# Optimization experiments

Hardware: AMD Instinct MI355X
Metric: run time of the kernel (lower is better)

## Reference

```python
import jax, jax.numpy as jnp
import numpy as np

QB = 127.0  # 2**(8-1) - 1


def ternary_dequant(w):
    # absmean ternary quantization, then dequantize by scale
    scale = jnp.mean(jnp.abs(w))
    w_t = jnp.clip(jnp.round(w / (scale + 1e-8)), -1.0, 1.0)
    w_t = jnp.where(scale == 0.0, jnp.zeros_like(w), w_t)
    return w_t * scale


def activation_quantize(x):
    # per-row (last-dim) absmax int8 fake-quant
    scale = jnp.max(jnp.abs(x), axis=-1, keepdims=True) / QB
    scale = jnp.maximum(scale, 1e-8)
    return jnp.clip(jnp.round(x / scale), -QB, QB) * scale


def setup_inputs() -> dict:
    key = jax.random.key(0)
    kx, kw = jax.random.split(key)
    x = jax.random.normal(kx, (2, 4096, 4096), dtype=jnp.float32)
    # kaiming_uniform-ish init scale; exact init distribution is irrelevant to the math
    bound = 1.0 / np.sqrt(4096)
    weight = jax.random.uniform(kw, (4096, 4096), dtype=jnp.float32,
                                minval=-bound, maxval=bound)
    return {"x": x, "weight": weight}


def reference(x, weight):
    w_q = ternary_dequant(weight)        # [out, in]
    x_q = activation_quantize(x)         # [b, s, in]
    return jnp.einsum('bsi,oi->bso', x_q, w_q)
```

## Files before the change

### kernel.cpp

```cpp
#include <hip/hip_runtime.h>
#include <stdint.h>
#include <stddef.h>


#define K_DIM 4096
#define M_DIM 8192
#define N_DIM 4096

typedef int v4i __attribute__((ext_vector_type(4)));

__device__ __forceinline__ void async_copy16(void* lds, const void* g) {
  __builtin_amdgcn_global_load_lds(
      (const __attribute__((address_space(1))) unsigned int*)g,
      (__attribute__((address_space(3))) unsigned int*)lds,
      16, 0, 0);
}

__global__ void k_wsum(const float* __restrict__ w, double* __restrict__ partials) {
  const float4* w4 = (const float4*)w;
  int tid = blockIdx.x * 256 + threadIdx.x;
  double s = 0.0;
  for (int i = tid; i < 4194304; i += 262144) {
    float4 v = w4[i];
    s += (double)fabsf(v.x) + (double)fabsf(v.y) +
         (double)fabsf(v.z) + (double)fabsf(v.w);
  }
  for (int off = 32; off > 0; off >>= 1) s += __shfl_down(s, off);
  __shared__ double lsum[4];
  int lane = threadIdx.x & 63, wid = threadIdx.x >> 6;
  if (lane == 0) lsum[wid] = s;
  __syncthreads();
  if (threadIdx.x == 0)
    partials[blockIdx.x] = lsum[0] + lsum[1] + lsum[2] + lsum[3];
}

__global__ void k_wq(const float* __restrict__ w, const double* __restrict__ partials,
                     float* __restrict__ wscale, char* __restrict__ qw) {
  __shared__ float sT;
  if (threadIdx.x < 64) {
    double s = 0.0;
    for (int i = threadIdx.x; i < 1024; i += 64) s += partials[i];
    for (int off = 32; off > 0; off >>= 1) s += __shfl_down(s, off);
    if (threadIdx.x == 0) {
      float sc = (float)(s / 16777216.0);
      if (blockIdx.x == 0) *wscale = sc;
      float d = sc + 1e-8f;
      unsigned lo = 1u, hi = __float_as_uint(d);
      while (hi - lo > 1u) {
        unsigned mid = lo + ((hi - lo) >> 1);
        if (__uint_as_float(mid) / d > 0.5f) hi = mid; else lo = mid;
      }
      sT = __uint_as_float(hi);
    }
  }
  __syncthreads();
  const float T = sT;
  const float4* w4 = (const float4*)w;
  int* q4 = (int*)qw;
  int tid = blockIdx.x * 256 + threadIdx.x;
  for (int i = tid; i < 4194304; i += 524288) {
    float4 v = w4[i];
    int a = (int)(v.x >= T) - (int)(v.x <= -T);
    int b = (int)(v.y >= T) - (int)(v.y <= -T);
    int c = (int)(v.z >= T) - (int)(v.z <= -T);
    int e = (int)(v.w >= T) - (int)(v.w <= -T);
    q4[i] = (a & 255) | ((b & 255) << 8) | ((c & 255) << 16) | ((e & 255) << 24);
  }
}

__global__ void k_xq(const float* __restrict__ x, char* __restrict__ qx,
                     float* __restrict__ sx) {
  int row = blockIdx.x;
  const float4* xr = (const float4*)(x + (size_t)row * K_DIM);
  float4 v[4];
  float m = 0.f;
#pragma unroll
  for (int c = 0; c < 4; c++) {
    v[c] = xr[threadIdx.x + c * 256];
    m = fmaxf(m, fmaxf(fmaxf(fabsf(v[c].x), fabsf(v[c].y)),
                       fmaxf(fabsf(v[c].z), fabsf(v[c].w))));
  }
  for (int off = 32; off > 0; off >>= 1) m = fmaxf(m, __shfl_down(m, off));
  __shared__ float lm[4];
  __shared__ float bscale;
  int lane = threadIdx.x & 63, wid = threadIdx.x >> 6;
  if (lane == 0) lm[wid] = m;
  __syncthreads();
  if (threadIdx.x == 0) {
    float mm = fmaxf(fmaxf(lm[0], lm[1]), fmaxf(lm[2], lm[3]));
    float sc = fmaxf(mm / 127.0f, 1e-8f);
    bscale = sc;
    sx[row] = sc;
  }
  __syncthreads();
  float sc = bscale;
  int* q4 = (int*)(qx + (size_t)row * K_DIM);
#pragma unroll
  for (int c = 0; c < 4; c++) {
    int a = (int)fmaxf(fminf(rintf(v[c].x / sc), 127.f), -127.f);
    int b = (int)fmaxf(fminf(rintf(v[c].y / sc), 127.f), -127.f);
    int cc = (int)fmaxf(fminf(rintf(v[c].z / sc), 127.f), -127.f);
    int e = (int)fmaxf(fminf(rintf(v[c].w / sc), 127.f), -127.f);
    q4[threadIdx.x + c * 256] = (a & 255) | ((b & 255) << 8) | ((cc & 255) << 16) | ((e & 255) << 24);
  }
}

__global__ __launch_bounds__(512, 2) void k_gemm(const char* __restrict__ qx,
                       const char* __restrict__ qw,
                       const float* __restrict__ sx,
                       const float* __restrict__ wscale,
                       float* __restrict__ out) {
  __shared__ char lds[4][32768];

  const int tid = threadIdx.x;
  const int lane = tid & 63;
  const int wave = tid >> 6;
  const int wr = wave >> 2;
  const int wc = wave & 3;

  const int wg = (blockIdx.x & 7) * 64 + (blockIdx.x >> 3);
  const int bm = wg >> 4;
  const int bn = wg & 15;
  const int rowBase = bm * 256;
  const int colBase = bn * 256;

  const int rl = tid >> 2;
  const int kswz = (((tid & 3) ^ ((rl >> 1) & 3)) << 4);
  const char* gA0 = qx + (size_t)(rowBase + rl) * K_DIM + kswz;
  const char* gA1 = gA0 + (size_t)128 * K_DIM;
  const char* gB0 = qw + (size_t)(colBase + rl) * K_DIM + kswz;
  const char* gB1 = gB0 + (size_t)128 * K_DIM;
  const int dOff = wave << 10;

  const int sR = ((lane & 15) >> 1) & 3;
  const int kro = (((lane >> 4) ^ sR) << 4);
  const int aOff = ((wr << 7) + (lane & 15)) * 64 + kro;
  const int bOff = 16384 + ((wc << 6) + (lane & 15)) * 64 + kro;

  v4i acc[8][4] = {};

  auto STAGE = [&](int t) {
    char* b = &lds[t & 3][0];
    const size_t ko = (size_t)t << 6;
    async_copy16(b + dOff,         gA0 + ko);
    async_copy16(b + 8192 + dOff,  gA1 + ko);
    async_copy16(b + 16384 + dOff, gB0 + ko);
    async_copy16(b + 24576 + dOff, gB1 + ko);
  };

  v4i afA[4], bfA[4], afB[4], bfB[4];

#define PRE_READ(T, AF, BF)                                                  \
  {                                                                          \
    const char* bx_ = &lds[(T) & 3][0];                                      \
    _Pragma("unroll") for (int j_ = 0; j_ < 4; ++j_)                         \
        BF[j_] = *(const v4i*)(bx_ + bOff + j_ * 1024);                      \
    _Pragma("unroll") for (int j_ = 0; j_ < 4; ++j_)                         \
        AF[j_] = *(const v4i*)(bx_ + aOff + j_ * 1024);                      \
  }

#define FULL_ITER(T, CURAF, CURBF, NXTAF, NXTBF, DO_STAGE, VMC)              \
  {                                                                          \
    asm volatile("s_waitcnt vmcnt(" #VMC ")" ::: "memory");                  \
    __builtin_amdgcn_s_barrier();                                            \
    asm volatile("" ::: "memory");                                           \
    const char* bc_ = &lds[(T) & 3][0];                                      \
    v4i afL_[4];                                                             \
    _Pragma("unroll") for (int j_ = 0; j_ < 4; ++j_)                         \
        afL_[j_] = *(const v4i*)(bc_ + aOff + (4 + j_) * 1024);              \
    PRE_READ((T) + 1, NXTAF, NXTBF);                                         \
    if (DO_STAGE) STAGE((T) + 3);                                            \
    asm volatile("" ::: "memory");                                           \
    __builtin_amdgcn_s_setprio(1);                                           \
    _Pragma("unroll") for (int m_ = 0; m_ < 4; ++m_)                         \
        _Pragma("unroll") for (int n_ = 0; n_ < 4; ++n_)                     \
            acc[m_][n_] = __builtin_amdgcn_mfma_i32_16x16x64_i8(             \
                CURAF[m_], CURBF[n_], acc[m_][n_], 0, 0, 0);                 \
    _Pragma("unroll") for (int m_ = 0; m_ < 4; ++m_)                         \
        _Pragma("unroll") for (int n_ = 0; n_ < 4; ++n_)                     \
            acc[4 + m_][n_] = __builtin_amdgcn_mfma_i32_16x16x64_i8(         \
                afL_[m_], CURBF[n_], acc[4 + m_][n_], 0, 0, 0);              \
    __builtin_amdgcn_s_setprio(0);                                           \
  }

  STAGE(0); STAGE(1); STAGE(2);
  asm volatile("s_waitcnt vmcnt(8)" ::: "memory");
  __builtin_amdgcn_s_barrier();
  asm volatile("" ::: "memory");
  PRE_READ(0, afA, bfA);

  for (int tp = 0; tp < 30; ++tp) {
    const int t = tp * 2;
    FULL_ITER(t,     afA, bfA, afB, bfB, 1, 4);
    FULL_ITER(t + 1, afB, bfB, afA, bfA, 1, 4);
  }
  FULL_ITER(60, afA, bfA, afB, bfB, 1, 4);
  FULL_ITER(61, afB, bfB, afA, bfA, 0, 4);
  FULL_ITER(62, afA, bfA, afB, bfB, 0, 0);
  {
    const char* bc_ = &lds[63 & 3][0];
    v4i afL_[4];
#pragma unroll
    for (int j_ = 0; j_ < 4; ++j_)
      afL_[j_] = *(const v4i*)(bc_ + aOff + (4 + j_) * 1024);
    __builtin_amdgcn_s_setprio(1);
#pragma unroll
    for (int m_ = 0; m_ < 4; ++m_)
#pragma unroll
      for (int n_ = 0; n_ < 4; ++n_)
        acc[m_][n_] = __builtin_amdgcn_mfma_i32_16x16x64_i8(
            afB[m_], bfB[n_], acc[m_][n_], 0, 0, 0);
#pragma unroll
    for (int m_ = 0; m_ < 4; ++m_)
#pragma unroll
      for (int n_ = 0; n_ < 4; ++n_)
        acc[4 + m_][n_] = __builtin_amdgcn_mfma_i32_16x16x64_i8(
            afL_[m_], bfB[n_], acc[4 + m_][n_], 0, 0, 0);
    __builtin_amdgcn_s_setprio(0);
  }
#undef FULL_ITER
#undef PRE_READ

  const float swv = *wscale;
  const int col0 = colBase + (wc << 6) + (lane & 15);
  const int row0 = rowBase + (wr << 7) + ((lane >> 4) << 2);
#pragma unroll
  for (int m = 0; m < 8; ++m) {
#pragma unroll
    for (int r = 0; r < 4; ++r) {
      const int row = row0 + m * 16 + r;
      const float s = sx[row] * swv;
#pragma unroll
      for (int n = 0; n < 4; ++n)
        out[(size_t)row * N_DIM + col0 + n * 16] = (float)acc[m][n][r] * s;
    }
  }
}

extern "C" void kernel_launch(void* const* d_in, const int* in_sizes, int n_in,
                              void* d_out, int out_size, void* d_ws, size_t ws_size,
                              hipStream_t stream) {
  const float* x = (const float*)d_in[0];
  const float* w = (const float*)d_in[1];
  float* out = (float*)d_out;
  char* ws = (char*)d_ws;

  double* partials = (double*)ws;
  float* wscale    = (float*)(ws + 8192);
  float* sx        = (float*)(ws + 8448);
  char*  qw        = ws + 41472;
  char*  qx        = ws + 41472 + 16777216;

  k_wsum<<<1024, 256, 0, stream>>>(w, partials);
  k_wq  <<<2048, 256, 0, stream>>>(w, partials, wscale, qw);
  k_xq  <<<8192, 256, 0, stream>>>(x, qx, sx);
  k_gemm<<<32 * 16, 512, 0, stream>>>(qx, qw, sx, wscale, out);
}
```

Measured before the change: 396.0 us.

## Load A fragments directly from global into registers, stage only B in LDS

The GEMM stops staging the activation (A) tile through LDS. Each wave now loads its A fragments straight from global memory into registers one k-step ahead, and only the weight (B) tile is streamed into LDS asynchronously. The wave layout changes from 2x4 to 4x2 so each wave owns 64 rows by 128 columns, reading 8 B fragments from LDS per step. This halves LDS footprint and LDS read traffic, but A loads become uncoalesced 16-byte per-lane global reads with less latency hiding, and the vmcnt accounting mixes the A loads with the async B copies.

```diff
diff --git a/kernel.cpp b/kernel.cpp
--- a/kernel.cpp
+++ b/kernel.cpp
@@ -110,13 +110,13 @@
                        const float* __restrict__ sx,
                        const float* __restrict__ wscale,
                        float* __restrict__ out) {
-  __shared__ char lds[4][32768];
+  __shared__ char lds[4][16384];
 
   const int tid = threadIdx.x;
   const int lane = tid & 63;
   const int wave = tid >> 6;
-  const int wr = wave >> 2;
-  const int wc = wave & 3;
+  const int wr = wave >> 1;
+  const int wc = wave & 1;
 
   const int wg = (blockIdx.x & 7) * 64 + (blockIdx.x >> 3);
   const int bm = wg >> 4;
@@ -126,112 +126,88 @@
 
   const int rl = tid >> 2;
   const int kswz = (((tid & 3) ^ ((rl >> 1) & 3)) << 4);
-  const char* gA0 = qx + (size_t)(rowBase + rl) * K_DIM + kswz;
-  const char* gA1 = gA0 + (size_t)128 * K_DIM;
   const char* gB0 = qw + (size_t)(colBase + rl) * K_DIM + kswz;
   const char* gB1 = gB0 + (size_t)128 * K_DIM;
   const int dOff = wave << 10;
 
   const int sR = ((lane & 15) >> 1) & 3;
   const int kro = (((lane >> 4) ^ sR) << 4);
-  const int aOff = ((wr << 7) + (lane & 15)) * 64 + kro;
-  const int bOff = 16384 + ((wc << 6) + (lane & 15)) * 64 + kro;
-
-  v4i acc[8][4] = {};
-
-  auto STAGE = [&](int t) {
+  const int bOff = ((wc << 7) + (lane & 15)) * 64 + kro;
+
+  const char* gAf = qx + (size_t)(rowBase + (wr << 6) + (lane & 15)) * K_DIM
+                       + ((lane >> 4) << 4);
+
+  v4i acc[4][8] = {};
+  v4i aA[4], aB[4];
+
+  auto STAGE_B = [&](int t) {
     char* b = &lds[t & 3][0];
     const size_t ko = (size_t)t << 6;
-    async_copy16(b + dOff,         gA0 + ko);
-    async_copy16(b + 8192 + dOff,  gA1 + ko);
-    async_copy16(b + 16384 + dOff, gB0 + ko);
-    async_copy16(b + 24576 + dOff, gB1 + ko);
+    async_copy16(b + dOff,        gB0 + ko);
+    async_copy16(b + 8192 + dOff, gB1 + ko);
   };
 
-  v4i afA[4], bfA[4], afB[4], bfB[4];
-
-#define PRE_READ(T, AF, BF)                                                  \
+#define A_LOAD(T, DST)                                                       \
   {                                                                          \
-    const char* bx_ = &lds[(T) & 3][0];                                      \
-    _Pragma("unroll") for (int j_ = 0; j_ < 4; ++j_)                         \
-        BF[j_] = *(const v4i*)(bx_ + bOff + j_ * 1024);                      \
-    _Pragma("unroll") for (int j_ = 0; j_ < 4; ++j_)                         \
-        AF[j_] = *(const v4i*)(bx_ + aOff + j_ * 1024);                      \
-  }
-
-#define FULL_ITER(T, CURAF, CURBF, NXTAF, NXTBF, DO_STAGE, VMC)              \
+    const char* ga_ = gAf + ((size_t)(T) << 6);                              \
+    _Pragma("unroll") for (int m_ = 0; m_ < 4; ++m_)                         \
+        DST[m_] = *(const v4i*)(ga_ + (size_t)m_ * 16 * K_DIM);              \
+  }
+
+#define BODY(T, CUR, NXT, DO_A, DO_STAGE)                                    \
   {                                                                          \
-    asm volatile("s_waitcnt vmcnt(" #VMC ")" ::: "memory");                  \
-    __builtin_amdgcn_s_barrier();                                            \
-    asm volatile("" ::: "memory");                                           \
-    const char* bc_ = &lds[(T) & 3][0];                                      \
-    v4i afL_[4];                                                             \
-    _Pragma("unroll") for (int j_ = 0; j_ < 4; ++j_)                         \
-        afL_[j_] = *(const v4i*)(bc_ + aOff + (4 + j_) * 1024);              \
-    PRE_READ((T) + 1, NXTAF, NXTBF);                                         \
-    if (DO_STAGE) STAGE((T) + 3);                                            \
+    const char* b_ = &lds[(T) & 3][0];                                       \
+    v4i bf_[8];                                                              \
+    _Pragma("unroll") for (int n_ = 0; n_ < 8; ++n_)                         \
+        bf_[n_] = *(const v4i*)(b_ + bOff + n_ * 1024);                      \
+    if (DO_A) A_LOAD((T) + 1, NXT);                                          \
+    if (DO_STAGE) STAGE_B((T) + 3);                                          \
     asm volatile("" ::: "memory");                                           \
     __builtin_amdgcn_s_setprio(1);                                           \
     _Pragma("unroll") for (int m_ = 0; m_ < 4; ++m_)                         \
-        _Pragma("unroll") for (int n_ = 0; n_ < 4; ++n_)                     \
+        _Pragma("unroll") for (int n_ = 0; n_ < 8; ++n_)                     \
             acc[m_][n_] = __builtin_amdgcn_mfma_i32_16x16x64_i8(             \
-                CURAF[m_], CURBF[n_], acc[m_][n_], 0, 0, 0);                 \
-    _Pragma("unroll") for (int m_ = 0; m_ < 4; ++m_)                         \
-        _Pragma("unroll") for (int n_ = 0; n_ < 4; ++n_)                     \
-            acc[4 + m_][n_] = __builtin_amdgcn_mfma_i32_16x16x64_i8(         \
-                afL_[m_], CURBF[n_], acc[4 + m_][n_], 0, 0, 0);              \
+                CUR[m_], bf_[n_], acc[m_][n_], 0, 0, 0);                     \
     __builtin_amdgcn_s_setprio(0);                                           \
   }
 
-  STAGE(0); STAGE(1); STAGE(2);
-  asm volatile("s_waitcnt vmcnt(8)" ::: "memory");
-  __builtin_amdgcn_s_barrier();
+#define WAIT_BAR(VMC)                                                        \
+  asm volatile("s_waitcnt vmcnt(" #VMC ")" ::: "memory");                    \
+  __builtin_amdgcn_s_barrier();                                              \
   asm volatile("" ::: "memory");
-  PRE_READ(0, afA, bfA);
-
+
+  STAGE_B(0); STAGE_B(1); STAGE_B(2);
+  A_LOAD(0, aA);
+  WAIT_BAR(0)
+
+  BODY(0, aA, aB, 1, 1)
   for (int tp = 0; tp < 30; ++tp) {
-    const int t = tp * 2;
-    FULL_ITER(t,     afA, bfA, afB, bfB, 1, 4);
-    FULL_ITER(t + 1, afB, bfB, afA, bfA, 1, 4);
-  }
-  FULL_ITER(60, afA, bfA, afB, bfB, 1, 4);
-  FULL_ITER(61, afB, bfB, afA, bfA, 0, 4);
-  FULL_ITER(62, afA, bfA, afB, bfB, 0, 0);
-  {
-    const char* bc_ = &lds[63 & 3][0];
-    v4i afL_[4];
-#pragma unroll
-    for (int j_ = 0; j_ < 4; ++j_)
-      afL_[j_] = *(const v4i*)(bc_ + aOff + (4 + j_) * 1024);
-    __builtin_amdgcn_s_setprio(1);
-#pragma unroll
-    for (int m_ = 0; m_ < 4; ++m_)
-#pragma unroll
-      for (int n_ = 0; n_ < 4; ++n_)
-        acc[m_][n_] = __builtin_amdgcn_mfma_i32_16x16x64_i8(
-            afB[m_], bfB[n_], acc[m_][n_], 0, 0, 0);
-#pragma unroll
-    for (int m_ = 0; m_ < 4; ++m_)
-#pragma unroll
-      for (int n_ = 0; n_ < 4; ++n_)
-        acc[4 + m_][n_] = __builtin_amdgcn_mfma_i32_16x16x64_i8(
-            afL_[m_], bfB[n_], acc[4 + m_][n_], 0, 0, 0);
-    __builtin_amdgcn_s_setprio(0);
-  }
-#undef FULL_ITER
-#undef PRE_READ
+    WAIT_BAR(2)
+    BODY(2 * tp + 1, aB, aA, 1, 1)
+    WAIT_BAR(2)
+    BODY(2 * tp + 2, aA, aB, 1, 1)
+  }
+  WAIT_BAR(2)
+  BODY(61, aB, aA, 1, 0)
+  WAIT_BAR(0)
+  BODY(62, aA, aB, 1, 0)
+  WAIT_BAR(0)
+  BODY(63, aB, aA, 0, 0)
+#undef BODY
+#undef A_LOAD
+#undef WAIT_BAR
 
   const float swv = *wscale;
-  const int col0 = colBase + (wc << 6) + (lane & 15);
-  const int row0 = rowBase + (wr << 7) + ((lane >> 4) << 2);
-#pragma unroll
-  for (int m = 0; m < 8; ++m) {
+  const int col0 = colBase + (wc << 7) + (lane & 15);
+  const int row0 = rowBase + (wr << 6) + ((lane >> 4) << 2);
+#pragma unroll
+  for (int m = 0; m < 4; ++m) {
 #pragma unroll
     for (int r = 0; r < 4; ++r) {
       const int row = row0 + m * 16 + r;
       const float s = sx[row] * swv;
 #pragma unroll
-      for (int n = 0; n < 4; ++n)
+      for (int n = 0; n < 8; ++n)
         out[(size_t)row * N_DIM + col0 + n * 16] = (float)acc[m][n][r] * s;
     }
   }
```

Result: slower. 471.2 us (+19.0%).
